# Performance work log

Measured on AMD Instinct MI355X. Metric: run time of the kernel, lower is better.

## Reference

```python
import jax, jax.numpy as jnp
import numpy as np
import math

PROJ_EPS = 0.001
C_CURV = 0.5  # hyperbolic curvature c


def setup_inputs() -> dict:
    key = jax.random.key(0)
    k1, k2, k3 = jax.random.split(key, 3)
    B, C, H, W, N = 4, 256, 256, 256, 19
    x = jax.random.normal(k1, (B, C, H, W), dtype=jnp.float32)
    # kaiming_uniform_(a=sqrt(5)) on (N, C): bound = sqrt(6 / ((1+5) * fan_in)) = 1/sqrt(C)
    bound = 1.0 / math.sqrt(C)
    P_MLR = jax.random.uniform(k2, (N, C), jnp.float32, -bound, bound)
    A_MLR = jax.random.uniform(k3, (N, C), jnp.float32, -bound, bound)
    return {"x": x, "P_MLR": P_MLR, "A_MLR": A_MLR}


def reference(x, P_MLR, A_MLR):
    K = jnp.float32(C_CURV)
    eps = jnp.float32(1e-12)

    xx = jnp.sum(x * x, axis=1)                       # (B,H,W)  ||x||^2
    pp = jnp.sum(P_MLR * P_MLR, axis=1)               # (N,)     ||-P||^2
    # 1x1 conv with kernel -P: channel contraction
    px = jnp.einsum('bchw,nc->bnhw', x, -P_MLR)       # (B,N,H,W)

    xx_b = xx[:, None]                                # (B,1,H,W)
    pp_b = pp[None, :, None, None]                    # (1,N,1,1)

    sqsq = (K * xx_b) * (K * pp_b)
    A = 1.0 + 2.0 * K * px + K * xx_b
    Bc = 1.0 - K * pp_b
    D = 1.0 + 2.0 * K * px + sqsq
    D = jnp.maximum(D, eps)
    alpha = A / D
    beta = Bc / D

    mobaddnorm = alpha * alpha * pp_b + beta * beta * xx_b + 2.0 * alpha * beta * px
    maxnorm = (1.0 - PROJ_EPS) / jnp.sqrt(K)
    sqrtm = jnp.sqrt(mobaddnorm)
    project_normalized = jnp.where(sqrtm > maxnorm,
                                   maxnorm / jnp.maximum(sqrtm, eps),
                                   jnp.ones_like(mobaddnorm))
    mobaddnormprojected = jnp.where(sqrtm < maxnorm, mobaddnorm,
                                    jnp.full_like(mobaddnorm, maxnorm * maxnorm))

    A_norm = jnp.linalg.norm(A_MLR, axis=1)           # (N,)
    normed_A = A_MLR / jnp.maximum(A_norm, eps)[:, None]  # torch F.normalize (eps=1e-12)

    xdota = beta * jnp.einsum('bchw,nc->bnhw', x, normed_A)
    pdota = alpha * jnp.sum(-P_MLR * normed_A, axis=1)[None, :, None, None]
    mobdota = (xdota + pdota) * project_normalized

    lamb_px = 2.0 / jnp.maximum(1.0 - K * mobaddnormprojected, eps)
    sineterm = jnp.sqrt(K) * mobdota * lamb_px
    out = (2.0 / jnp.sqrt(K)) * A_norm[None, :, None, None] * jnp.arcsinh(sineterm)
    return out
```

## Files before the change

kernel.cpp:

```cpp
#include <hip/hip_runtime.h>
#include <math.h>

#define C_DIM 256
#define N_DIM 19
#define HW 65536
#define PP_OFF (N_DIM * C_DIM)
#define PA_OFF (PP_OFF + 32)
#define AN_OFF (PP_OFF + 64)

__global__ void prep_kernel(const float* __restrict__ P,
                            const float* __restrict__ A,
                            float* __restrict__ ws) {
    int n = blockIdx.x;
    int lane = threadIdx.x;
    float pp = 0.f, aa = 0.f, pa = 0.f;
    for (int c = lane; c < C_DIM; c += 64) {
        float p = P[n * C_DIM + c];
        float a = A[n * C_DIM + c];
        pp += p * p;
        aa += a * a;
        pa += p * a;
    }
#pragma unroll
    for (int off = 32; off > 0; off >>= 1) {
        pp += __shfl_xor(pp, off);
        aa += __shfl_xor(aa, off);
        pa += __shfl_xor(pa, off);
    }
    float an  = sqrtf(aa);
    float inv = 1.0f / fmaxf(an, 1e-12f);
    for (int c = lane; c < C_DIM; c += 64) {
        ws[n * C_DIM + c] = A[n * C_DIM + c] * inv;
    }
    if (lane == 0) {
        ws[PP_OFF + n] = pp;
        ws[PA_OFF + n] = -pa * inv;
        ws[AN_OFF + n] = an;
    }
}

__global__ __launch_bounds__(256) void hyper_mlr_main(
    const float* __restrict__ x, const float* __restrict__ P,
    const float* __restrict__ ws, float* __restrict__ out)
{
    __shared__ float sP[N_DIM * C_DIM];
    __shared__ float sA[N_DIM * C_DIM];
    for (int i = threadIdx.x; i < N_DIM * C_DIM; i += 256) {
        sP[i] = -P[i];
        sA[i] = ws[i];
    }
    __syncthreads();

    int tid = blockIdx.x * 256 + threadIdx.x;
    int s   = tid * 2;
    int b   = s >> 16;
    int hw  = s & 65535;
    const float* xb = x + (size_t)b * C_DIM * HW + hw;

    float xx0 = 0.f, xx1 = 0.f;
    float px0[N_DIM], px1[N_DIM], xa0[N_DIM], xa1[N_DIM];
#pragma unroll
    for (int n = 0; n < N_DIM; ++n) { px0[n] = px1[n] = xa0[n] = xa1[n] = 0.f; }

#pragma unroll 4
    for (int c = 0; c < C_DIM; c += 2) {
        float2 v0 = *reinterpret_cast<const float2*>(xb + (size_t)c * HW);
        float2 v1 = *reinterpret_cast<const float2*>(xb + (size_t)(c + 1) * HW);
        xx0 += v0.x * v0.x; xx0 += v1.x * v1.x;
        xx1 += v0.y * v0.y; xx1 += v1.y * v1.y;
#pragma unroll
        for (int n = 0; n < N_DIM; ++n) {
            float2 p = *reinterpret_cast<const float2*>(&sP[n * C_DIM + c]);
            float2 a = *reinterpret_cast<const float2*>(&sA[n * C_DIM + c]);
            px0[n] += v0.x * p.x; px0[n] += v1.x * p.y;
            px1[n] += v0.y * p.x; px1[n] += v1.y * p.y;
            xa0[n] += v0.x * a.x; xa0[n] += v1.x * a.y;
            xa1[n] += v0.y * a.x; xa1[n] += v1.y * a.y;
        }
    }

    const float K        = 0.5f;
    const float sqK      = 0.70710678118654752f;
    const float maxnorm  = 0.999f / sqK;
    const float maxnorm2 = maxnorm * maxnorm;
    const float eps      = 1e-12f;

    float* ob = out + (size_t)b * N_DIM * HW + hw;
#pragma unroll
    for (int n = 0; n < N_DIM; ++n) {
        float pp = ws[PP_OFF + n];
        float pa = ws[PA_OFF + n];
        float an = ws[AN_OFF + n];
        float o0, o1;
        float pxs0 = px0[n], pxs1 = px1[n];
        float xas0 = xa0[n], xas1 = xa1[n];
        {
            float px = pxs0, xa = xas0, xx = xx0;
            float Av = 1.0f + px + K * xx;
            float Bv = 1.0f - K * pp;
            float D  = fmaxf(1.0f + px + (K * K) * xx * pp, eps);
            float alpha = Av / D, beta = Bv / D;
            float mob = alpha * alpha * pp + beta * beta * xx + 2.0f * alpha * beta * px;
            float sqrtm = sqrtf(fmaxf(mob, 0.0f));
            float proj = (sqrtm > maxnorm) ? (maxnorm / fmaxf(sqrtm, eps)) : 1.0f;
            float mobp = (sqrtm < maxnorm) ? mob : maxnorm2;
            float mobdota = (beta * xa + alpha * pa) * proj;
            float lamb = 2.0f / fmaxf(1.0f - K * mobp, eps);
            float sine = sqK * mobdota * lamb;
            o0 = (2.0f / sqK) * an * asinhf(sine);
        }
        {
            float px = pxs1, xa = xas1, xx = xx1;
            float Av = 1.0f + px + K * xx;
            float Bv = 1.0f - K * pp;
            float D  = fmaxf(1.0f + px + (K * K) * xx * pp, eps);
            float alpha = Av / D, beta = Bv / D;
            float mob = alpha * alpha * pp + beta * beta * xx + 2.0f * alpha * beta * px;
            float sqrtm = sqrtf(fmaxf(mob, 0.0f));
            float proj = (sqrtm > maxnorm) ? (maxnorm / fmaxf(sqrtm, eps)) : 1.0f;
            float mobp = (sqrtm < maxnorm) ? mob : maxnorm2;
            float mobdota = (beta * xa + alpha * pa) * proj;
            float lamb = 2.0f / fmaxf(1.0f - K * mobp, eps);
            float sine = sqK * mobdota * lamb;
            o1 = (2.0f / sqK) * an * asinhf(sine);
        }
        *reinterpret_cast<float2*>(ob + (size_t)n * HW) = make_float2(o0, o1);
    }
}

extern "C" void kernel_launch(void* const* d_in, const int* in_sizes, int n_in,
                              void* d_out, int out_size, void* d_ws, size_t ws_size,
                              hipStream_t stream) {
    const float* x  = (const float*)d_in[0];
    const float* P  = (const float*)d_in[1];
    const float* A  = (const float*)d_in[2];
    float* out = (float*)d_out;
    float* ws  = (float*)d_ws;

    prep_kernel<<<N_DIM, 64, 0, stream>>>(P, A, ws);
    hyper_mlr_main<<<512, 256, 0, stream>>>(x, P, ws, out);
}
```

Baseline: 500.2 us.

## Use one pixel per thread with float4 LDS weights and register prefetch

Each thread now handles one pixel instead of two, which halves the accumulator registers, and the grid doubles to 1024 blocks with launch bounds asking for 4 blocks per CU. Weights are read from shared memory as float4 over four channels, and the next four channels of x are loaded into registers one step ahead. The per-class constants are cached in shared memory instead of read from global memory. The aim is more occupancy and better latency hiding on the memory-bound x stream. In exchange, each weight read from LDS is reused over one pixel instead of two, and global loads drop from float2 to scalar.

```diff
diff --git a/kernel.cpp b/kernel.cpp
--- a/kernel.cpp
+++ b/kernel.cpp
@@ -4,6 +4,7 @@
 #define C_DIM 256
 #define N_DIM 19
 #define HW 65536
+#define CQ 64
 #define PP_OFF (N_DIM * C_DIM)
 #define PA_OFF (PP_OFF + 32)
 #define AN_OFF (PP_OFF + 64)
@@ -39,43 +40,70 @@
     }
 }
 
-__global__ __launch_bounds__(256) void hyper_mlr_main(
+__global__ __launch_bounds__(256, 4) void hyper_mlr_main(
     const float* __restrict__ x, const float* __restrict__ P,
     const float* __restrict__ ws, float* __restrict__ out)
 {
-    __shared__ float sP[N_DIM * C_DIM];
-    __shared__ float sA[N_DIM * C_DIM];
-    for (int i = threadIdx.x; i < N_DIM * C_DIM; i += 256) {
-        sP[i] = -P[i];
-        sA[i] = ws[i];
+    __shared__ float4 sP4[N_DIM * CQ];
+    __shared__ float4 sA4[N_DIM * CQ];
+    __shared__ float  spp[N_DIM], spa[N_DIM], san[N_DIM];
+
+    const float4* P4 = reinterpret_cast<const float4*>(P);
+    const float4* W4 = reinterpret_cast<const float4*>(ws);
+    for (int i = threadIdx.x; i < N_DIM * CQ; i += 256) {
+        float4 pv = P4[i];
+        sP4[i] = make_float4(-pv.x, -pv.y, -pv.z, -pv.w);
+        sA4[i] = W4[i];
+    }
+    if (threadIdx.x < N_DIM) {
+        spp[threadIdx.x] = ws[PP_OFF + threadIdx.x];
+        spa[threadIdx.x] = ws[PA_OFF + threadIdx.x];
+        san[threadIdx.x] = ws[AN_OFF + threadIdx.x];
     }
     __syncthreads();
 
     int tid = blockIdx.x * 256 + threadIdx.x;
-    int s   = tid * 2;
-    int b   = s >> 16;
-    int hw  = s & 65535;
+    int b   = tid >> 16;
+    int hw  = tid & 65535;
     const float* xb = x + (size_t)b * C_DIM * HW + hw;
 
-    float xx0 = 0.f, xx1 = 0.f;
-    float px0[N_DIM], px1[N_DIM], xa0[N_DIM], xa1[N_DIM];
+    float xx = 0.f;
+    float px[N_DIM], xa[N_DIM];
 #pragma unroll
-    for (int n = 0; n < N_DIM; ++n) { px0[n] = px1[n] = xa0[n] = xa1[n] = 0.f; }
+    for (int n = 0; n < N_DIM; ++n) { px[n] = 0.f; xa[n] = 0.f; }
 
-#pragma unroll 4
-    for (int c = 0; c < C_DIM; c += 2) {
-        float2 v0 = *reinterpret_cast<const float2*>(xb + (size_t)c * HW);
-        float2 v1 = *reinterpret_cast<const float2*>(xb + (size_t)(c + 1) * HW);
-        xx0 += v0.x * v0.x; xx0 += v1.x * v1.x;
-        xx1 += v0.y * v0.y; xx1 += v1.y * v1.y;
+    float x0 = xb[0];
+    float x1 = xb[(size_t)HW];
+    float x2 = xb[(size_t)2 * HW];
+    float x3 = xb[(size_t)3 * HW];
+
+#pragma unroll 2
+    for (int cq = 0; cq < CQ - 1; ++cq) {
+        const float* xn = xb + (size_t)(cq + 1) * 4 * HW;
+        float n0 = xn[0];
+        float n1 = xn[(size_t)HW];
+        float n2 = xn[(size_t)2 * HW];
+        float n3 = xn[(size_t)3 * HW];
+
+        xx += x0 * x0; xx += x1 * x1; xx += x2 * x2; xx += x3 * x3;
 #pragma unroll
         for (int n = 0; n < N_DIM; ++n) {
-            float2 p = *reinterpret_cast<const float2*>(&sP[n * C_DIM + c]);
-            float2 a = *reinterpret_cast<const float2*>(&sA[n * C_DIM + c]);
-            px0[n] += v0.x * p.x; px0[n] += v1.x * p.y;
-            px1[n] += v0.y * p.x; px1[n] += v1.y * p.y;
-            xa0[n] += v0.x * a.x; xa0[n] += v1.x * a.y;
-            xa1[n] += v0.y * a.x; xa1[n] += v1.y * a.y;
+            float4 p = sP4[n * CQ + cq];
+            float4 a = sA4[n * CQ + cq];
+            px[n] += x0 * p.x; px[n] += x1 * p.y; px[n] += x2 * p.z; px[n] += x3 * p.w;
+            xa[n] += x0 * a.x; xa[n] += x1 * a.y; xa[n] += x2 * a.z; xa[n] += x3 * a.w;
+        }
+        x0 = n0; x1 = n1; x2 = n2; x3 = n3;
+    }
+    {
+        const int cq = CQ - 1;
+        xx += x0 * x0; xx += x1 * x1; xx += x2 * x2; xx += x3 * x3;
+#pragma unroll
+        for (int n = 0; n < N_DIM; ++n) {
+            float4 p = sP4[n * CQ + cq];
+            float4 a = sA4[n * CQ + cq];
+            px[n] += x0 * p.x; px[n] += x1 * p.y; px[n] += x2 * p.z; px[n] += x3 * p.w;
+            xa[n] += x0 * a.x; xa[n] += x1 * a.y; xa[n] += x2 * a.z; xa[n] += x3 * a.w;
         }
     }
 
@@ -88,43 +116,23 @@
     float* ob = out + (size_t)b * N_DIM * HW + hw;
 #pragma unroll
     for (int n = 0; n < N_DIM; ++n) {
-        float pp = ws[PP_OFF + n];
-        float pa = ws[PA_OFF + n];
-        float an = ws[AN_OFF + n];
-        float o0, o1;
-        float pxs0 = px0[n], pxs1 = px1[n];
-        float xas0 = xa0[n], xas1 = xa1[n];
-        {
-            float px = pxs0, xa = xas0, xx = xx0;
-            float Av = 1.0f + px + K * xx;
-            float Bv = 1.0f - K * pp;
-            float D  = fmaxf(1.0f + px + (K * K) * xx * pp, eps);
-            float alpha = Av / D, beta = Bv / D;
-            float mob = alpha * alpha * pp + beta * beta * xx + 2.0f * alpha * beta * px;
-            float sqrtm = sqrtf(fmaxf(mob, 0.0f));
-            float proj = (sqrtm > maxnorm) ? (maxnorm / fmaxf(sqrtm, eps)) : 1.0f;
-            float mobp = (sqrtm < maxnorm) ? mob : maxnorm2;
-            float mobdota = (beta * xa + alpha * pa) * proj;
-            float lamb = 2.0f / fmaxf(1.0f - K * mobp, eps);
-            float sine = sqK * mobdota * lamb;
-            o0 = (2.0f / sqK) * an * asinhf(sine);
-        }
-        {
-            float px = pxs1, xa = xas1, xx = xx1;
-            float Av = 1.0f + px + K * xx;
-            float Bv = 1.0f - K * pp;
-            float D  = fmaxf(1.0f + px + (K * K) * xx * pp, eps);
-            float alpha = Av / D, beta = Bv / D;
-            float mob = alpha * alpha * pp + beta * beta * xx + 2.0f * alpha * beta * px;
-            float sqrtm = sqrtf(fmaxf(mob, 0.0f));
-            float proj = (sqrtm > maxnorm) ? (maxnorm / fmaxf(sqrtm, eps)) : 1.0f;
-            float mobp = (sqrtm < maxnorm) ? mob : maxnorm2;
-            float mobdota = (beta * xa + alpha * pa) * proj;
-            float lamb = 2.0f / fmaxf(1.0f - K * mobp, eps);
-            float sine = sqK * mobdota * lamb;
-            o1 = (2.0f / sqK) * an * asinhf(sine);
-        }
-        *reinterpret_cast<float2*>(ob + (size_t)n * HW) = make_float2(o0, o1);
+        float pp = spp[n];
+        float pa = spa[n];
+        float an = san[n];
+        float pxs = px[n], xas = xa[n];
+
+        float Av = 1.0f + pxs + K * xx;
+        float Bv = 1.0f - K * pp;
+        float D  = fmaxf(1.0f + pxs + (K * K) * xx * pp, eps);
+        float alpha = Av / D, beta = Bv / D;
+        float mob = alpha * alpha * pp + beta * beta * xx + 2.0f * alpha * beta * pxs;
+        float sqrtm = sqrtf(fmaxf(mob, 0.0f));
+        float proj = (sqrtm > maxnorm) ? (maxnorm / fmaxf(sqrtm, eps)) : 1.0f;
+        float mobp = (sqrtm < maxnorm) ? mob : maxnorm2;
+        float mobdota = (beta * xas + alpha * pa) * proj;
+        float lamb = 2.0f / fmaxf(1.0f - K * mobp, eps);
+        float sine = sqK * mobdota * lamb;
+        ob[(size_t)n * HW] = (2.0f / sqK) * an * asinhf(sine);
     }
 }
 
@@ -138,5 +146,5 @@
     float* ws  = (float*)d_ws;
 
     prep_kernel<<<N_DIM, 64, 0, stream>>>(P, A, ws);
-    hyper_mlr_main<<<512, 256, 0, stream>>>(x, P, ws, out);
+    hyper_mlr_main<<<1024, 256, 0, stream>>>(x, P, ws, out);
 }
```

Result: faster. 434.6 us (-13.1%).
